# Optimization experiments

Measured on AMD Instinct MI355X. Metric: run time of the kernel, lower is better.

Reference implementation:

```python
import jax, jax.numpy as jnp
import numpy as np

VOCAB, EMBED, HIDDEN = 32000, 256, 512
N, L = 64, 2048

def setup_inputs() -> dict:
    key = jax.random.key(0)
    k1, k2, k3, k4 = jax.random.split(key, 4)
    X = jax.random.randint(k1, (N, L), 0, VOCAB)
    E = jax.random.normal(k2, (VOCAB, EMBED), dtype=jnp.float32) * 0.02
    W_hh = jax.random.normal(k3, (HIDDEN, HIDDEN), dtype=jnp.float32) / np.sqrt(HIDDEN)
    b_hh = jnp.zeros((HIDDEN,), dtype=jnp.float32)
    W_xh = jax.random.normal(k4, (EMBED, HIDDEN), dtype=jnp.float32) / np.sqrt(EMBED)
    b_xh = jnp.zeros((HIDDEN,), dtype=jnp.float32)
    return {"X": X, "E": E, "W_hh": W_hh, "b_hh": b_hh, "W_xh": W_xh, "b_xh": b_xh}

def reference(X, E, W_hh, b_hh, W_xh, b_xh):
    # Embed tokens: (N, L, De)
    xe = E[X]
    # Precompute input projection for all timesteps in one big GEMM: (N, L, H)
    xp = jnp.einsum('nld,dh->nlh', xe, W_xh) + b_xh
    h0 = jnp.zeros((X.shape[0], W_hh.shape[0]), dtype=E.dtype)

    def step(h, x_t):
        # h: (N, H); x_t: (N, H) already projected
        h_new = jnp.tanh(h @ W_hh + b_hh + x_t)
        return h_new, None

    # scan over time: move L to leading axis -> (L, N, H)
    h_last, _ = jax.lax.scan(step, h0, jnp.swapaxes(xp, 0, 1))
    return h_last
```

## Files before the change

### kernel.cpp

```cpp
#include <hip/hip_runtime.h>

typedef _Float16 h8 __attribute__((ext_vector_type(8)));
typedef float f4v __attribute__((ext_vector_type(4)));
typedef unsigned int u32;
typedef unsigned long long u64;
typedef u32 u32x4 __attribute__((ext_vector_type(4)));

#define SEQ 2048
#define HID 512
#define EMB 256
#define NV 32000
#define LOSCALE 2048.0f
#define INV_LOSCALE 4.8828125e-4f

#define WS_WHI 0u
#define WS_WLO (512u * 1024u)
#define WS_HG (1024u * 1024u)
#define WS_FLAGS (WS_HG + 256u * 1024u)
#define WS_PROJ (WS_FLAGS + 4u * 1024u)
#define FLAG_STRIDE 32

__global__ void wsplit_kernel(const float* __restrict__ Whh,
                              _Float16* __restrict__ Whi,
                              _Float16* __restrict__ Wlo) {
  int gid = blockIdx.x * 256 + threadIdx.x;
  int l = gid & 63, c = gid >> 6;
  int kb = c & 15, jtg = c >> 4;
  int j = jtg * 16 + (l & 15);
  int k0 = kb * 32 + (l >> 4) * 8;
  _Float16 hi[8], lo[8];
#pragma unroll
  for (int e = 0; e < 8; ++e) {
    float v = Whh[(k0 + e) * HID + j];
    _Float16 h = (_Float16)v;
    hi[e] = h;
    lo[e] = (_Float16)((v - (float)h) * LOSCALE);
  }
  *(h8*)(Whi + (size_t)gid * 8) = *(const h8*)hi;
  *(h8*)(Wlo + (size_t)gid * 8) = *(const h8*)lo;
}

template <bool PF32>
__global__ __launch_bounds__(256) void proj_kernel(const float* __restrict__ E,
                                                   const float* __restrict__ Wxh,
                                                   const float* __restrict__ bxh,
                                                   void* __restrict__ projE) {
  __shared__ float El[32 * EMB];
  const int t = threadIdx.x;
  const int v0 = blockIdx.x * 32;
  {
    const float4* src = (const float4*)(E + (size_t)v0 * EMB);
    float4* dst = (float4*)El;
#pragma unroll
    for (int i = 0; i < 8; ++i) dst[t + i * 256] = src[t + i * 256];
  }
  __syncthreads();
  const int c0 = (t & 63) * 8;
  const int rg = t >> 6;
  float acc[8][8];
#pragma unroll
  for (int r = 0; r < 8; ++r)
#pragma unroll
    for (int c = 0; c < 8; ++c) acc[r][c] = 0.f;

#pragma unroll 4
  for (int d = 0; d < EMB; ++d) {
    float wv[8];
    *(float4*)&wv[0] = *(const float4*)&Wxh[d * HID + c0];
    *(float4*)&wv[4] = *(const float4*)&Wxh[d * HID + c0 + 4];
#pragma unroll
    for (int r = 0; r < 8; ++r) {
      float ev = El[(rg * 8 + r) * EMB + d];
#pragma unroll
      for (int c = 0; c < 8; ++c) acc[r][c] = fmaf(ev, wv[c], acc[r][c]);
    }
  }
  float bv[8];
  *(float4*)&bv[0] = *(const float4*)&bxh[c0];
  *(float4*)&bv[4] = *(const float4*)&bxh[c0 + 4];
#pragma unroll
  for (int r = 0; r < 8; ++r) {
    int row = v0 + rg * 8 + r;
    if (PF32) {
      float o[8];
#pragma unroll
      for (int c = 0; c < 8; ++c) o[c] = acc[r][c] + bv[c];
      *(float4*)((float*)projE + (size_t)row * HID + c0) = *(const float4*)&o[0];
      *(float4*)((float*)projE + (size_t)row * HID + c0 + 4) = *(const float4*)&o[4];
    } else {
      _Float16 o[8];
#pragma unroll
      for (int c = 0; c < 8; ++c) o[c] = (_Float16)(acc[r][c] + bv[c]);
      *(h8*)((_Float16*)projE + (size_t)row * HID + c0) = *(const h8*)o;
    }
  }
}

__global__ void init_kernel(float4* __restrict__ p) {
  int gid = blockIdx.x * 256 + threadIdx.x;
  if (gid < 16640) p[gid] = (float4){0.f, 0.f, 0.f, 0.f};
}

template <bool PF32>
__global__ __launch_bounds__(512, 2) void rnn_kernel(
    const int* __restrict__ X, const _Float16* __restrict__ Whi,
    const _Float16* __restrict__ Wlo, const void* __restrict__ projE,
    const float* __restrict__ bhh, u32* __restrict__ hX,
    u32* __restrict__ flags, float* __restrict__ out) {
  __shared__ u32 hs[8192];
  const int tid = threadIdx.x;
  const int w = tid >> 6, lane = tid & 63;
  const int g = lane >> 4, li = lane & 15;
  const int grp = blockIdx.x >> 2, cb = blockIdx.x & 3;
  const int nb = grp * 16;
  const int jtg = cb * 8 + w;
  const int j = jtg * 16 + li;

  h8 Wh[16], Wl[16];
  {
    const char* wb = (const char*)Whi + ((size_t)jtg * 16 * 64 + lane) * 16;
    const char* wb2 = (const char*)Wlo + ((size_t)jtg * 16 * 64 + lane) * 16;
#pragma unroll
    for (int kb = 0; kb < 16; ++kb) {
      Wh[kb] = *(const h8*)(wb + (size_t)kb * 1024);
      Wl[kb] = *(const h8*)(wb2 + (size_t)kb * 1024);
    }
  }
  const float bias = bhh[j];
  u32* fl = flags + grp * 4 * FLAG_STRIDE;

  const int gq = ((jtg & 1) << 1) | (li >> 3);
  const int pubbase = (jtg >> 1) * 512 + ((li >> 2) & 1) * 256 +
                      (gq * 16 + g * 4) * 4 + (li & 3);
  u32* const hgrp = hX + grp * 8192;

  for (int t = 0; t < SEQ; ++t) {
    float pv[4];
#pragma unroll
    for (int i = 0; i < 4; ++i) {
      int tok = X[(nb + g * 4 + i) * SEQ + t];
      if (PF32)
        pv[i] = ((const float*)projE)[(size_t)tok * HID + j];
      else
        pv[i] = (float)((const _Float16*)projE)[(size_t)tok * HID + j];
    }

    if (t > 0 && lane < 4) {
      u32 spins = 0;
      while (__hip_atomic_load(fl + lane * FLAG_STRIDE, __ATOMIC_RELAXED,
                               __HIP_MEMORY_SCOPE_AGENT) < (u32)t) {
        if (++spins > 10000u) break;
      }
    }

    {
      const u32* src = hgrp + (t & 1) * 32768;
      u64 v[4][2];
#pragma unroll
      for (int q = 0; q < 4; ++q) {
        int idx = tid * 4 + q * 2048;
        v[q][0] = __hip_atomic_load((const u64*)(src + idx), __ATOMIC_RELAXED,
                                    __HIP_MEMORY_SCOPE_AGENT);
        v[q][1] = __hip_atomic_load((const u64*)(src + idx + 2),
                                    __ATOMIC_RELAXED, __HIP_MEMORY_SCOPE_AGENT);
      }
#pragma unroll
      for (int q = 0; q < 4; ++q) {
        u32x4 d;
        d[0] = (u32)v[q][0]; d[1] = (u32)(v[q][0] >> 32);
        d[2] = (u32)v[q][1]; d[3] = (u32)(v[q][1] >> 32);
        *(u32x4*)(hs + tid * 4 + q * 2048) = d;
      }
    }
    __syncthreads();

    f4v a1 = {0.f, 0.f, 0.f, 0.f};
    f4v c1 = {0.f, 0.f, 0.f, 0.f};
    f4v c2 = {0.f, 0.f, 0.f, 0.f};
#pragma unroll
    for (int kb = 0; kb < 16; ++kb) {
      u32x4 p0 = *(const u32x4*)(hs + kb * 512 + lane * 4);
      u32x4 p1 = *(const u32x4*)(hs + kb * 512 + 256 + lane * 4);
      u32 hiw[4], low[4];
      hiw[0] = (p0[0] & 0xFFFFu) | (p0[1] << 16);
      hiw[1] = (p0[2] & 0xFFFFu) | (p0[3] << 16);
      hiw[2] = (p1[0] & 0xFFFFu) | (p1[1] << 16);
      hiw[3] = (p1[2] & 0xFFFFu) | (p1[3] << 16);
      low[0] = (p0[0] >> 16) | (p0[1] & 0xFFFF0000u);
      low[1] = (p0[2] >> 16) | (p0[3] & 0xFFFF0000u);
      low[2] = (p1[0] >> 16) | (p1[1] & 0xFFFF0000u);
      low[3] = (p1[2] >> 16) | (p1[3] & 0xFFFF0000u);
      h8 ahc = *(const h8*)hiw;
      h8 alc = *(const h8*)low;
      a1 = __builtin_amdgcn_mfma_f32_16x16x32_f16(ahc, Wh[kb], a1, 0, 0, 0);
      c1 = __builtin_amdgcn_mfma_f32_16x16x32_f16(ahc, Wl[kb], c1, 0, 0, 0);
      c2 = __builtin_amdgcn_mfma_f32_16x16x32_f16(alc, Wh[kb], c2, 0, 0, 0);
    }

    u32* const hn = hgrp + ((t + 1) & 1) * 32768;
    const bool lastt = (t == SEQ - 1);
#pragma unroll
    for (int i = 0; i < 4; ++i) {
      float v = a1[i] + INV_LOSCALE * (c1[i] + c2[i]) + bias + pv[i];
      float e2 = __expf(2.0f * v);
      float th = 1.0f - 2.0f / (e2 + 1.0f);
      _Float16 hh = (_Float16)th;
      _Float16 hl = (_Float16)((th - (float)hh) * LOSCALE);
      u32 packed = (u32)__builtin_bit_cast(unsigned short, hh) |
                   ((u32)__builtin_bit_cast(unsigned short, hl) << 16);
      __hip_atomic_store(hn + pubbase + i * 4, packed, __ATOMIC_RELAXED,
                         __HIP_MEMORY_SCOPE_AGENT);
      if (lastt) out[(nb + g * 4 + i) * HID + j] = th;
    }
    __syncthreads();
    if (tid == 0) {
      __hip_atomic_store(fl + cb * FLAG_STRIDE, (u32)(t + 1), __ATOMIC_RELAXED,
                         __HIP_MEMORY_SCOPE_AGENT);
    }
  }
}

extern "C" void kernel_launch(void* const* d_in, const int* in_sizes, int n_in,
                              void* d_out, int out_size, void* d_ws,
                              size_t ws_size, hipStream_t stream) {
  const int* X = (const int*)d_in[0];
  const float* E = (const float*)d_in[1];
  const float* Whh = (const float*)d_in[2];
  const float* bhh = (const float*)d_in[3];
  const float* Wxh = (const float*)d_in[4];
  const float* bxh = (const float*)d_in[5];
  float* out = (float*)d_out;

  char* ws = (char*)d_ws;
  _Float16* Whi = (_Float16*)(ws + WS_WHI);
  _Float16* Wlo = (_Float16*)(ws + WS_WLO);
  u32* hX = (u32*)(ws + WS_HG);
  u32* flags = (u32*)(ws + WS_FLAGS);
  void* projE = (void*)(ws + WS_PROJ);
  const bool pf32 = ws_size >= (size_t)WS_PROJ + (size_t)NV * HID * sizeof(float);

  wsplit_kernel<<<128, 256, 0, stream>>>(Whh, Whi, Wlo);
  init_kernel<<<65, 256, 0, stream>>>((float4*)(ws + WS_HG));
  if (pf32) {
    proj_kernel<true><<<NV / 32, 256, 0, stream>>>(E, Wxh, bxh, projE);
    rnn_kernel<true><<<16, 512, 0, stream>>>(X, Whi, Wlo, projE, bhh, hX, flags, out);
  } else {
    proj_kernel<false><<<NV / 32, 256, 0, stream>>>(E, Wxh, bxh, projE);
    rnn_kernel<false><<<16, 512, 0, stream>>>(X, Whi, Wlo, projE, bhh, hX, flags, out);
  }
}
```

Baseline: 7.522 ms.

## Publish hidden state pre-split into hi/lo fp16 planes to drop per-step unpacking

Hidden-state publication now uses a lane shuffle to pair neighbouring outputs, so each stored word already holds two hi halves or two lo halves, laid out as separate hi and lo planes. The MFMA inner loop can then load its h8 operands directly from shared memory instead of loading interleaved words and repacking them with shifts and masks every step. The change also pins the weight registers with an empty asm barrier and hoists the per-row token pointers. It adds one cross-lane shuffle per output and depends on the new publish layout matching the consumer's read layout exactly.

New measurement: 6.248 ms. 16.9% less time.

```diff
diff --git a/kernel.cpp b/kernel.cpp
--- a/kernel.cpp
+++ b/kernel.cpp
@@ -125,20 +125,33 @@
       Wh[kb] = *(const h8*)(wb + (size_t)kb * 1024);
       Wl[kb] = *(const h8*)(wb2 + (size_t)kb * 1024);
     }
+#pragma unroll
+    for (int kb = 0; kb < 16; ++kb) {
+      f4v th = __builtin_bit_cast(f4v, Wh[kb]);
+      f4v tl = __builtin_bit_cast(f4v, Wl[kb]);
+      asm volatile("" : "+v"(th), "+v"(tl));
+      Wh[kb] = __builtin_bit_cast(h8, th);
+      Wl[kb] = __builtin_bit_cast(h8, tl);
+    }
   }
   const float bias = bhh[j];
   u32* fl = flags + grp * 4 * FLAG_STRIDE;
 
-  const int gq = ((jtg & 1) << 1) | (li >> 3);
-  const int pubbase = (jtg >> 1) * 512 + ((li >> 2) & 1) * 256 +
-                      (gq * 16 + g * 4) * 4 + (li & 3);
+  const int hi2 = ((jtg & 1) << 1) | (li >> 3);
+  const int pub0 = (li & 1) * 4096 + (jtg >> 1) * 256 + (hi2 << 6) + g * 16 +
+                   ((li & 7) >> 1);
   u32* const hgrp = hX + grp * 8192;
+  const bool oddli = (li & 1) != 0;
+
+  const int* Xr[4];
+#pragma unroll
+  for (int i = 0; i < 4; ++i) Xr[i] = X + (size_t)(nb + g * 4 + i) * SEQ;
 
   for (int t = 0; t < SEQ; ++t) {
     float pv[4];
 #pragma unroll
     for (int i = 0; i < 4; ++i) {
-      int tok = X[(nb + g * 4 + i) * SEQ + t];
+      int tok = Xr[i][t];
       if (PF32)
         pv[i] = ((const float*)projE)[(size_t)tok * HID + j];
       else
@@ -177,21 +190,12 @@
     f4v a1 = {0.f, 0.f, 0.f, 0.f};
     f4v c1 = {0.f, 0.f, 0.f, 0.f};
     f4v c2 = {0.f, 0.f, 0.f, 0.f};
+    const u32* hb_hi = hs + lane * 4;
+    const u32* hb_lo = hs + 4096 + lane * 4;
 #pragma unroll
     for (int kb = 0; kb < 16; ++kb) {
-      u32x4 p0 = *(const u32x4*)(hs + kb * 512 + lane * 4);
-      u32x4 p1 = *(const u32x4*)(hs + kb * 512 + 256 + lane * 4);
-      u32 hiw[4], low[4];
-      hiw[0] = (p0[0] & 0xFFFFu) | (p0[1] << 16);
-      hiw[1] = (p0[2] & 0xFFFFu) | (p0[3] << 16);
-      hiw[2] = (p1[0] & 0xFFFFu) | (p1[1] << 16);
-      hiw[3] = (p1[2] & 0xFFFFu) | (p1[3] << 16);
-      low[0] = (p0[0] >> 16) | (p0[1] & 0xFFFF0000u);
-      low[1] = (p0[2] >> 16) | (p0[3] & 0xFFFF0000u);
-      low[2] = (p1[0] >> 16) | (p1[1] & 0xFFFF0000u);
-      low[3] = (p1[2] >> 16) | (p1[3] & 0xFFFF0000u);
-      h8 ahc = *(const h8*)hiw;
-      h8 alc = *(const h8*)low;
+      h8 ahc = *(const h8*)(hb_hi + kb * 256);
+      h8 alc = *(const h8*)(hb_lo + kb * 256);
       a1 = __builtin_amdgcn_mfma_f32_16x16x32_f16(ahc, Wh[kb], a1, 0, 0, 0);
       c1 = __builtin_amdgcn_mfma_f32_16x16x32_f16(ahc, Wl[kb], c1, 0, 0, 0);
       c2 = __builtin_amdgcn_mfma_f32_16x16x32_f16(alc, Wh[kb], c2, 0, 0, 0);
@@ -206,9 +210,12 @@
       float th = 1.0f - 2.0f / (e2 + 1.0f);
       _Float16 hh = (_Float16)th;
       _Float16 hl = (_Float16)((th - (float)hh) * LOSCALE);
-      u32 packed = (u32)__builtin_bit_cast(unsigned short, hh) |
-                   ((u32)__builtin_bit_cast(unsigned short, hl) << 16);
-      __hip_atomic_store(hn + pubbase + i * 4, packed, __ATOMIC_RELAXED,
+      u32 pk = (u32)__builtin_bit_cast(unsigned short, hh) |
+               ((u32)__builtin_bit_cast(unsigned short, hl) << 16);
+      u32 nbv = (u32)__shfl_xor((int)pk, 1, 64);
+      u32 word = oddli ? ((nbv >> 16) | (pk & 0xFFFF0000u))
+                       : ((pk & 0xFFFFu) | (nbv << 16));
+      __hip_atomic_store(hn + pub0 + i * 4, word, __ATOMIC_RELAXED,
                          __HIP_MEMORY_SCOPE_AGENT);
       if (lastt) out[(nb + g * 4 + i) * HID + j] = th;
     }
```
